# Performance work log

Measured on AMD Instinct MI355X. Metric: run time of the kernel, lower is better.

## Reference

```python
import jax, jax.numpy as jnp
import numpy as np

D_MODEL = 1024
N_EXPERTS = 8
TOP_K = 2


def setup_inputs() -> dict:
    key = jax.random.key(0)
    k1, k2, k3, k4 = jax.random.split(key, 4)
    B, S, D, E = 4, 2048, D_MODEL, N_EXPERTS
    dff = 4 * D
    # xavier-uniform style scale for expert weights
    lim = float(np.sqrt(6.0 / (D + dff)))
    return {
        "x": jax.random.normal(k1, (B, S, D), dtype=jnp.float32),
        "router_w": jax.random.normal(k2, (D, E), dtype=jnp.float32) * (1.0 / np.sqrt(D)),
        "router_b": jnp.zeros((E,), dtype=jnp.float32),
        "expert_up": jax.random.uniform(k3, (E, dff, D), dtype=jnp.float32, minval=-lim, maxval=lim),
        "expert_down": jax.random.uniform(k4, (E, D, dff), dtype=jnp.float32, minval=-lim, maxval=lim),
    }


def reference(x, router_w, router_b, expert_up, expert_down):
    B, S, D = x.shape
    E = expert_up.shape[0]
    x_flat = x.reshape(-1, D)                       # [T, D]
    logits = x_flat @ router_w + router_b           # [T, E]
    probs = jax.nn.softmax(logits, axis=-1)
    top_w, top_idx = jax.lax.top_k(probs, TOP_K)    # [T, K]
    # combine per-token top-k weights into a dense [T, E] combine matrix
    comb = jnp.sum(top_w[..., None] * jax.nn.one_hot(top_idx, E, dtype=x.dtype), axis=1)  # [T, E]
    output = jnp.zeros_like(x_flat)
    for e in range(E):  # fixed small expert count
        h = jax.nn.gelu(x_flat @ expert_up[e].T, approximate=False)   # [T, dff]
        out_e = h @ expert_down[e].T                                  # [T, D]
        output = output + comb[:, e:e + 1] * out_e
    return output.reshape(B, S, D)
```

## Files before the change

### kernel.cpp

```cpp
#include <hip/hip_runtime.h>
#include <hip/hip_bf16.h>
#include <cstdint>

#define T_TOK 8192
#define DM 1024
#define NE 8
#define DFF 4096

#define PERX_UP 576
#define PERX_DN 288

typedef __attribute__((ext_vector_type(8))) short bf16x8;
typedef __attribute__((ext_vector_type(4))) float f32x4;

__device__ __forceinline__ unsigned short f2bf(float f) {
  unsigned int b = __float_as_uint(f);
  b += 0x7FFFu + ((b >> 16) & 1u);
  return (unsigned short)(b >> 16);
}

__device__ __forceinline__ float gelu_exact(float v) {
  return 0.5f * v * (1.0f + erff(v * 0.70710678118654752440f));
}

__global__ void cvt_kernel(const float* __restrict__ x, unsigned short* __restrict__ xb) {
  size_t i = (size_t)blockIdx.x * blockDim.x + threadIdx.x;
  const f32x4* p = (const f32x4*)x;
  f32x4 a = p[2 * i];
  f32x4 b = p[2 * i + 1];
  union { bf16x8 v; unsigned short u[8]; } o;
  o.u[0] = f2bf(a.x); o.u[1] = f2bf(a.y); o.u[2] = f2bf(a.z); o.u[3] = f2bf(a.w);
  o.u[4] = f2bf(b.x); o.u[5] = f2bf(b.y); o.u[6] = f2bf(b.z); o.u[7] = f2bf(b.w);
  ((bf16x8*)xb)[i] = o.v;
}

__global__ void router_kernel(const float* __restrict__ x, const float* __restrict__ rw,
                              const float* __restrict__ rb, int* __restrict__ counts,
                              int* __restrict__ tlist, float* __restrict__ wlist) {
  const int lane = threadIdx.x & 63;
  const int t = blockIdx.x * 4 + (threadIdx.x >> 6);
  const float* xr = x + (size_t)t * DM;
  float acc[NE];
#pragma unroll
  for (int e = 0; e < NE; ++e) acc[e] = 0.0f;
#pragma unroll
  for (int i = 0; i < 16; ++i) {
    int d = lane + i * 64;
    float xv = xr[d];
    const float* wr = rw + (size_t)d * NE;
#pragma unroll
    for (int e = 0; e < NE; ++e) acc[e] = fmaf(xv, wr[e], acc[e]);
  }
#pragma unroll
  for (int off = 32; off; off >>= 1) {
#pragma unroll
    for (int e = 0; e < NE; ++e) acc[e] += __shfl_xor(acc[e], off);
  }
  float m = -1e30f;
#pragma unroll
  for (int e = 0; e < NE; ++e) { acc[e] += rb[e]; m = fmaxf(m, acc[e]); }
  float p[NE]; float s = 0.0f;
#pragma unroll
  for (int e = 0; e < NE; ++e) { p[e] = expf(acc[e] - m); s += p[e]; }
  int e1 = 0; float p1 = p[0];
#pragma unroll
  for (int e = 1; e < NE; ++e) if (p[e] > p1) { p1 = p[e]; e1 = e; }
  int e2 = -1; float p2 = -1e30f;
#pragma unroll
  for (int e = 0; e < NE; ++e) if (e != e1 && p[e] > p2) { p2 = p[e]; e2 = e; }
  float inv = 1.0f / s;
  if (lane == 0) {
    int r1 = atomicAdd(counts + e1, 1);
    tlist[e1 * T_TOK + r1] = t; wlist[e1 * T_TOK + r1] = p1 * inv;
    int r2 = atomicAdd(counts + e2, 1);
    tlist[e2 * T_TOK + r2] = t; wlist[e2 * T_TOK + r2] = p2 * inv;
  }
}

__global__ void prefix_kernel(const int* __restrict__ counts, int* __restrict__ offs,
                              int* __restrict__ wl_up, int* __restrict__ wl_dn) {
  __shared__ int te[144], tr[144], sn;
  if (threadIdx.x == 0) {
    int s = 0, n = 0;
    for (int e = 0; e < NE; ++e) {
      offs[e] = s; s += counts[e];
      int ntile = (counts[e] + 127) / 128;
      for (int r = 0; r < ntile; ++r) { te[n] = e; tr[n] = r; ++n; }
    }
    sn = n;
  }
  __syncthreads();
  const int n = sn;
  for (int idx = threadIdx.x; idx < 8 * PERX_UP; idx += blockDim.x) {
    int k = idx / PERX_UP, i = idx % PERX_UP;
    int g0 = (n * k) / 8, g1 = (n * (k + 1)) / 8, gc = g1 - g0;
    int v = -1;
    if (gc > 0 && i < 32 * gc) {
      int ct = i / gc, g = g0 + i % gc;
      v = (te[g] << 24) | (tr[g] << 16) | ct;
    }
    wl_up[idx] = v;
  }
  for (int idx = threadIdx.x; idx < 8 * PERX_DN; idx += blockDim.x) {
    int k = idx / PERX_DN, i = idx % PERX_DN;
    int g0 = (n * k) / 8, g1 = (n * (k + 1)) / 8, gc = g1 - g0;
    int v = -1;
    if (gc > 0 && i < 16 * gc) {
      int kh = i / (8 * gc);
      int rem = i % (8 * gc);
      int ct = rem / gc, g = g0 + rem % gc;
      v = (te[g] << 24) | (tr[g] << 16) | (kh << 8) | ct;
    }
    wl_dn[idx] = v;
  }
}

#define GL2LDS16(g, l) \
  __builtin_amdgcn_global_load_lds((const __attribute__((address_space(1))) unsigned int*)(g), \
                                   (__attribute__((address_space(3))) unsigned int*)(l), 16, 0, 0)

#define VMCNT4   asm volatile("s_waitcnt vmcnt(4)" ::: "memory")
#define VMCNT0   asm volatile("s_waitcnt vmcnt(0)" ::: "memory")
#define LGKM0    asm volatile("s_waitcnt lgkmcnt(0)" ::: "memory")
#define BARRIER() do { asm volatile("" ::: "memory"); __builtin_amdgcn_s_barrier(); asm volatile("" ::: "memory"); } while (0)

#define STAGE(bi, t) do { \
  const int k_ = (t) * 32; \
  GL2LDS16(asrc0 + k_, smem + (bi) * 4096 + wv * 512); \
  GL2LDS16(asrc1 + k_, smem + (bi) * 4096 + wv * 512 + 2048); \
  GL2LDS16(bsrc0 + k_, smem + 8192 + (bi) * 4096 + wv * 512); \
  GL2LDS16(bsrc1 + k_, smem + 8192 + (bi) * 4096 + wv * 512 + 2048); \
} while (0)

#define COMPUTE(bi) do { \
  const unsigned short* sA_ = smem + (bi) * 4096; \
  const unsigned short* sB_ = smem + 8192 + (bi) * 4096; \
  bf16x8 af_[4], bf_[4]; \
  _Pragma("unroll") \
  for (int m_ = 0; m_ < 4; ++m_) af_[m_] = *(const bf16x8*)(sA_ + (wr + m_ * 16 + lr) * 32 + kx); \
  _Pragma("unroll") \
  for (int n_ = 0; n_ < 4; ++n_) bf_[n_] = *(const bf16x8*)(sB_ + (wc + n_ * 16 + lr) * 32 + kx); \
  _Pragma("unroll") \
  for (int m_ = 0; m_ < 4; ++m_) \
    _Pragma("unroll") \
    for (int n_ = 0; n_ < 4; ++n_) \
      acc[m_][n_] = __builtin_amdgcn_mfma_f32_16x16x32_bf16(af_[m_], bf_[n_], acc[m_][n_], 0, 0, 0); \
} while (0)

#define KLOOP(NT) do { \
  STAGE(0, 0); \
  STAGE(1, 1); \
  for (int t = 0; t < (NT); ++t) { \
    const int b_ = t & 1; \
    if (t + 1 < (NT)) { VMCNT4; } else { VMCNT0; } \
    BARRIER(); \
    COMPUTE(b_); \
    if (t + 2 < (NT)) { \
      LGKM0; \
      BARRIER(); \
      STAGE(b_, t + 2); \
    } \
  } \
} while (0)

__global__ __launch_bounds__(256, 4) void gemm_up_kernel(
    const unsigned short* __restrict__ xb, const unsigned short* __restrict__ wb,
    const int* __restrict__ counts, const int* __restrict__ offs,
    const int* __restrict__ wl, const int* __restrict__ tlist,
    unsigned short* __restrict__ h) {
  const int xcd = blockIdx.x & 7, slot = blockIdx.x >> 3;
  const int item = wl[xcd * PERX_UP + slot];
  if (item < 0) return;
  const int e = (item >> 24) & 7, rt = (item >> 16) & 0xFF, ct = item & 0xFF;
  const int cnt = counts[e];

  __shared__ unsigned short smem[16384];

  const int tid = threadIdx.x;
  const int wv = tid >> 6, ln = tid & 63;
  const int swz = (tid & 3) ^ ((tid >> 3) & 3);

  const int arow = wv * 16 + (ln >> 2);
  int r0 = rt * 128 + arow;
  int r1 = r0 + 64;
  const int tok0 = tlist[e * T_TOK + (r0 < cnt ? r0 : cnt - 1)];
  const int tok1 = tlist[e * T_TOK + (r1 < cnt ? r1 : cnt - 1)];
  const unsigned short* asrc0 = xb + (size_t)tok0 * DM + swz * 8;
  const unsigned short* asrc1 = xb + (size_t)tok1 * DM + swz * 8;

  const unsigned short* bsrc0 =
      wb + (size_t)e * DFF * DM + (size_t)(ct * 128 + arow) * DM + swz * 8;
  const unsigned short* bsrc1 = bsrc0 + (size_t)64 * DM;

  const int wr = (wv >> 1) * 64, wc = (wv & 1) * 64;
  const int lr = ln & 15;
  const int kx = (((ln >> 4) ^ ((lr >> 1) & 3))) * 8;

  f32x4 acc[4][4] = {};

  KLOOP(DM / 32);

  BARRIER();

  unsigned short* sH = smem;
#pragma unroll
  for (int m = 0; m < 4; ++m) {
    int rloc = wr + m * 16 + (ln >> 4) * 4;
#pragma unroll
    for (int j = 0; j < 4; ++j) {
      int row = rloc + j;
#pragma unroll
      for (int n = 0; n < 4; ++n) {
        int col = wc + n * 16 + lr;
        int sl = ((col >> 3) ^ (row & 7)) * 8 + (col & 7);
        sH[row * 128 + sl] = f2bf(gelu_exact(acc[m][n][j]));
      }
    }
  }
  __syncthreads();
  const size_t hbase = (size_t)offs[e];
#pragma unroll
  for (int it = 0; it < 8; ++it) {
    int idx = it * 256 + tid;
    int row = idx >> 4, c8 = idx & 15;
    if (rt * 128 + row < cnt) {
      unsigned short* hp = h + (hbase + rt * 128 + row) * (size_t)DFF + ct * 128 + c8 * 8;
      *(bf16x8*)hp = *(const bf16x8*)&sH[row * 128 + (c8 ^ (row & 7)) * 8];
    }
  }
}

__global__ __launch_bounds__(256, 4) void gemm_down_kernel(
    const unsigned short* __restrict__ h, const unsigned short* __restrict__ wb,
    const int* __restrict__ counts, const int* __restrict__ offs,
    const int* __restrict__ wl, const int* __restrict__ tlist,
    const float* __restrict__ wlist, float* __restrict__ out) {
  const int xcd = blockIdx.x & 7, slot = blockIdx.x >> 3;
  const int item = wl[xcd * PERX_DN + slot];
  if (item < 0) return;
  const int e = (item >> 24) & 7, rt = (item >> 16) & 0xFF;
  const int kh = (item >> 8) & 1, ct = item & 0xFF;
  const int cnt = counts[e];

  __shared__ unsigned short smem[16384];

  const int tid = threadIdx.x;
  const int wv = tid >> 6, ln = tid & 63;
  const int swz = (tid & 3) ^ ((tid >> 3) & 3);
  const size_t hbase = (size_t)offs[e];
  const int kbase = kh * (DFF / 2);

  const int arow = wv * 16 + (ln >> 2);
  int r0 = rt * 128 + arow;
  int r1 = r0 + 64;
  const unsigned short* asrc0 =
      h + (hbase + (r0 < cnt ? r0 : cnt - 1)) * (size_t)DFF + kbase + swz * 8;
  const unsigned short* asrc1 =
      h + (hbase + (r1 < cnt ? r1 : cnt - 1)) * (size_t)DFF + kbase + swz * 8;

  const unsigned short* bsrc0 =
      wb + (size_t)e * DM * DFF + (size_t)(ct * 128 + arow) * DFF + kbase + swz * 8;
  const unsigned short* bsrc1 = bsrc0 + (size_t)64 * DFF;

  const int wr = (wv >> 1) * 64, wc = (wv & 1) * 64;
  const int lr = ln & 15;
  const int kx = (((ln >> 4) ^ ((lr >> 1) & 3))) * 8;

  f32x4 acc[4][4] = {};

  KLOOP(DFF / 2 / 32);

#pragma unroll
  for (int m = 0; m < 4; ++m) {
    int rloc = wr + m * 16 + (ln >> 4) * 4;
#pragma unroll
    for (int j = 0; j < 4; ++j) {
      int row = rt * 128 + rloc + j;
      if (row < cnt) {
        int tok = tlist[e * T_TOK + row];
        float w = wlist[e * T_TOK + row];
        float* op = out + (size_t)tok * DM + ct * 128 + wc + lr;
#pragma unroll
        for (int n = 0; n < 4; ++n) atomicAdd(op + n * 16, w * acc[m][n][j]);
      }
    }
  }
}

extern "C" void kernel_launch(void* const* d_in, const int* in_sizes, int n_in,
                              void* d_out, int out_size, void* d_ws, size_t ws_size,
                              hipStream_t stream) {
  const float* x  = (const float*)d_in[0];
  const float* rw = (const float*)d_in[1];
  const float* rb = (const float*)d_in[2];
  const float* up = (const float*)d_in[3];
  const float* dn = (const float*)d_in[4];
  float* out = (float*)d_out;
  char* ws = (char*)d_ws;

  int*   counts = (int*)(ws + 0);
  int*   offs   = (int*)(ws + 128);
  int*   wl_up  = (int*)(ws + 4096);
  int*   wl_dn  = (int*)(ws + 24576);
  int*   tlist  = (int*)(ws + 65536);
  float* wlist  = (float*)(ws + 65536 + 262144);
  unsigned short* xb = (unsigned short*)(ws + 589824);
  unsigned short* h  = (unsigned short*)(ws + 17367040);
  unsigned short* wbuf = (unsigned short*)(ws + 151584768);

  hipMemsetAsync(counts, 0, 64, stream);
  hipMemsetAsync(d_out, 0, (size_t)T_TOK * DM * sizeof(float), stream);

  cvt_kernel<<<dim3((T_TOK * DM / 8) / 256), 256, 0, stream>>>(x, xb);
  router_kernel<<<dim3(T_TOK / 4), 256, 0, stream>>>(x, rw, rb, counts, tlist, wlist);
  prefix_kernel<<<dim3(1), 256, 0, stream>>>(counts, offs, wl_up, wl_dn);

  cvt_kernel<<<dim3((NE * DFF * DM / 8) / 256), 256, 0, stream>>>(up, wbuf);
  gemm_up_kernel<<<dim3(8 * PERX_UP), 256, 0, stream>>>(xb, wbuf, counts, offs, wl_up, tlist, h);

  cvt_kernel<<<dim3((NE * DM * DFF / 8) / 256), 256, 0, stream>>>(dn, wbuf);
  gemm_down_kernel<<<dim3(8 * PERX_DN), 256, 0, stream>>>(h, wbuf, counts, offs, wl_dn, tlist, wlist, out);
}
```

Measured before the change: 700.6 us.

## Widen GEMM tiles to 128x256 and use triple-buffered LDS pipeline

Both expert GEMMs now compute 128x256 output tiles instead of 128x128, so each wave holds a 64x128 accumulator and the weight tile is reused across more tokens. The work lists are halved to match. The K loop moves from double to triple buffering, which lets one barrier per iteration replace the lgkmcnt wait plus second barrier before restaging. The cost is more LDS (72KB) and registers per block, with occupancy dropped to 2 blocks per CU, and fewer blocks to spread load across the device.

```diff
diff --git a/kernel.cpp b/kernel.cpp
--- a/kernel.cpp
+++ b/kernel.cpp
@@ -7,8 +7,8 @@
 #define NE 8
 #define DFF 4096
 
-#define PERX_UP 576
-#define PERX_DN 288
+#define PERX_UP 288
+#define PERX_DN 144
 
 typedef __attribute__((ext_vector_type(8))) short bf16x8;
 typedef __attribute__((ext_vector_type(4))) float f32x4;
@@ -95,7 +95,7 @@
     int k = idx / PERX_UP, i = idx % PERX_UP;
     int g0 = (n * k) / 8, g1 = (n * (k + 1)) / 8, gc = g1 - g0;
     int v = -1;
-    if (gc > 0 && i < 32 * gc) {
+    if (gc > 0 && i < 16 * gc) {
       int ct = i / gc, g = g0 + i % gc;
       v = (te[g] << 24) | (tr[g] << 16) | ct;
     }
@@ -105,9 +105,9 @@
     int k = idx / PERX_DN, i = idx % PERX_DN;
     int g0 = (n * k) / 8, g1 = (n * (k + 1)) / 8, gc = g1 - g0;
     int v = -1;
-    if (gc > 0 && i < 16 * gc) {
-      int kh = i / (8 * gc);
-      int rem = i % (8 * gc);
+    if (gc > 0 && i < 8 * gc) {
+      int kh = i / (4 * gc);
+      int rem = i % (4 * gc);
       int ct = rem / gc, g = g0 + rem % gc;
       v = (te[g] << 24) | (tr[g] << 16) | (kh << 8) | ct;
     }
@@ -119,51 +119,50 @@
   __builtin_amdgcn_global_load_lds((const __attribute__((address_space(1))) unsigned int*)(g), \
                                    (__attribute__((address_space(3))) unsigned int*)(l), 16, 0, 0)
 
-#define VMCNT4   asm volatile("s_waitcnt vmcnt(4)" ::: "memory")
+#define VMCNT6   asm volatile("s_waitcnt vmcnt(6)" ::: "memory")
 #define VMCNT0   asm volatile("s_waitcnt vmcnt(0)" ::: "memory")
-#define LGKM0    asm volatile("s_waitcnt lgkmcnt(0)" ::: "memory")
 #define BARRIER() do { asm volatile("" ::: "memory"); __builtin_amdgcn_s_barrier(); asm volatile("" ::: "memory"); } while (0)
 
 #define STAGE(bi, t) do { \
   const int k_ = (t) * 32; \
   GL2LDS16(asrc0 + k_, smem + (bi) * 4096 + wv * 512); \
-  GL2LDS16(asrc1 + k_, smem + (bi) * 4096 + wv * 512 + 2048); \
-  GL2LDS16(bsrc0 + k_, smem + 8192 + (bi) * 4096 + wv * 512); \
-  GL2LDS16(bsrc1 + k_, smem + 8192 + (bi) * 4096 + wv * 512 + 2048); \
+  GL2LDS16(asrc1 + k_, smem + (bi) * 4096 + 2048 + wv * 512); \
+  GL2LDS16(bsrc0 + k_, smem + 12288 + (bi) * 8192 + wv * 512); \
+  GL2LDS16(bsrc1 + k_, smem + 12288 + (bi) * 8192 + 2048 + wv * 512); \
+  GL2LDS16(bsrc2 + k_, smem + 12288 + (bi) * 8192 + 4096 + wv * 512); \
+  GL2LDS16(bsrc3 + k_, smem + 12288 + (bi) * 8192 + 6144 + wv * 512); \
 } while (0)
 
 #define COMPUTE(bi) do { \
   const unsigned short* sA_ = smem + (bi) * 4096; \
-  const unsigned short* sB_ = smem + 8192 + (bi) * 4096; \
-  bf16x8 af_[4], bf_[4]; \
+  const unsigned short* sB_ = smem + 12288 + (bi) * 8192; \
+  bf16x8 af_[4], bf_[8]; \
   _Pragma("unroll") \
   for (int m_ = 0; m_ < 4; ++m_) af_[m_] = *(const bf16x8*)(sA_ + (wr + m_ * 16 + lr) * 32 + kx); \
   _Pragma("unroll") \
-  for (int n_ = 0; n_ < 4; ++n_) bf_[n_] = *(const bf16x8*)(sB_ + (wc + n_ * 16 + lr) * 32 + kx); \
+  for (int n_ = 0; n_ < 8; ++n_) bf_[n_] = *(const bf16x8*)(sB_ + (wc + n_ * 16 + lr) * 32 + kx); \
   _Pragma("unroll") \
   for (int m_ = 0; m_ < 4; ++m_) \
     _Pragma("unroll") \
-    for (int n_ = 0; n_ < 4; ++n_) \
+    for (int n_ = 0; n_ < 8; ++n_) \
       acc[m_][n_] = __builtin_amdgcn_mfma_f32_16x16x32_bf16(af_[m_], bf_[n_], acc[m_][n_], 0, 0, 0); \
 } while (0)
 
 #define KLOOP(NT) do { \
   STAGE(0, 0); \
   STAGE(1, 1); \
+  int bc_ = 0, bs_ = 2; \
   for (int t = 0; t < (NT); ++t) { \
-    const int b_ = t & 1; \
-    if (t + 1 < (NT)) { VMCNT4; } else { VMCNT0; } \
+    if (t + 1 < (NT)) { VMCNT6; } else { VMCNT0; } \
     BARRIER(); \
-    COMPUTE(b_); \
-    if (t + 2 < (NT)) { \
-      LGKM0; \
-      BARRIER(); \
-      STAGE(b_, t + 2); \
-    } \
+    COMPUTE(bc_); \
+    if (t + 2 < (NT)) STAGE(bs_, t + 2); \
+    bc_ = (bc_ == 2) ? 0 : bc_ + 1; \
+    bs_ = (bs_ == 2) ? 0 : bs_ + 1; \
   } \
 } while (0)
 
-__global__ __launch_bounds__(256, 4) void gemm_up_kernel(
+__global__ __launch_bounds__(256, 2) void gemm_up_kernel(
     const unsigned short* __restrict__ xb, const unsigned short* __restrict__ wb,
     const int* __restrict__ counts, const int* __restrict__ offs,
     const int* __restrict__ wl, const int* __restrict__ tlist,
@@ -174,29 +173,30 @@
   const int e = (item >> 24) & 7, rt = (item >> 16) & 0xFF, ct = item & 0xFF;
   const int cnt = counts[e];
 
-  __shared__ unsigned short smem[16384];
+  __shared__ unsigned short smem[36864];
 
   const int tid = threadIdx.x;
   const int wv = tid >> 6, ln = tid & 63;
-  const int swz = (tid & 3) ^ ((tid >> 3) & 3);
-
-  const int arow = wv * 16 + (ln >> 2);
-  int r0 = rt * 128 + arow;
-  int r1 = r0 + 64;
-  const int tok0 = tlist[e * T_TOK + (r0 < cnt ? r0 : cnt - 1)];
-  const int tok1 = tlist[e * T_TOK + (r1 < cnt ? r1 : cnt - 1)];
+  const int srow = wv * 16 + (ln >> 2);
+  const int swz = (ln & 3) ^ ((ln >> 3) & 3);
+
+  int ra0 = rt * 128 + srow, ra1 = ra0 + 64;
+  const int tok0 = tlist[e * T_TOK + (ra0 < cnt ? ra0 : cnt - 1)];
+  const int tok1 = tlist[e * T_TOK + (ra1 < cnt ? ra1 : cnt - 1)];
   const unsigned short* asrc0 = xb + (size_t)tok0 * DM + swz * 8;
   const unsigned short* asrc1 = xb + (size_t)tok1 * DM + swz * 8;
 
   const unsigned short* bsrc0 =
-      wb + (size_t)e * DFF * DM + (size_t)(ct * 128 + arow) * DM + swz * 8;
+      wb + (size_t)e * DFF * DM + (size_t)(ct * 256 + srow) * DM + swz * 8;
   const unsigned short* bsrc1 = bsrc0 + (size_t)64 * DM;
-
-  const int wr = (wv >> 1) * 64, wc = (wv & 1) * 64;
+  const unsigned short* bsrc2 = bsrc0 + (size_t)128 * DM;
+  const unsigned short* bsrc3 = bsrc0 + (size_t)192 * DM;
+
+  const int wr = (wv >> 1) * 64, wc = (wv & 1) * 128;
   const int lr = ln & 15;
   const int kx = (((ln >> 4) ^ ((lr >> 1) & 3))) * 8;
 
-  f32x4 acc[4][4] = {};
+  f32x4 acc[4][8] = {};
 
   KLOOP(DM / 32);
 
@@ -210,27 +210,27 @@
     for (int j = 0; j < 4; ++j) {
       int row = rloc + j;
 #pragma unroll
-      for (int n = 0; n < 4; ++n) {
+      for (int n = 0; n < 8; ++n) {
         int col = wc + n * 16 + lr;
         int sl = ((col >> 3) ^ (row & 7)) * 8 + (col & 7);
-        sH[row * 128 + sl] = f2bf(gelu_exact(acc[m][n][j]));
+        sH[row * 256 + sl] = f2bf(gelu_exact(acc[m][n][j]));
       }
     }
   }
   __syncthreads();
   const size_t hbase = (size_t)offs[e];
 #pragma unroll
-  for (int it = 0; it < 8; ++it) {
+  for (int it = 0; it < 16; ++it) {
     int idx = it * 256 + tid;
-    int row = idx >> 4, c8 = idx & 15;
+    int row = idx >> 5, c8 = idx & 31;
     if (rt * 128 + row < cnt) {
-      unsigned short* hp = h + (hbase + rt * 128 + row) * (size_t)DFF + ct * 128 + c8 * 8;
-      *(bf16x8*)hp = *(const bf16x8*)&sH[row * 128 + (c8 ^ (row & 7)) * 8];
-    }
-  }
-}
-
-__global__ __launch_bounds__(256, 4) void gemm_down_kernel(
+      unsigned short* hp = h + (hbase + rt * 128 + row) * (size_t)DFF + ct * 256 + c8 * 8;
+      *(bf16x8*)hp = *(const bf16x8*)&sH[row * 256 + (c8 ^ (row & 7)) * 8];
+    }
+  }
+}
+
+__global__ __launch_bounds__(256, 2) void gemm_down_kernel(
     const unsigned short* __restrict__ h, const unsigned short* __restrict__ wb,
     const int* __restrict__ counts, const int* __restrict__ offs,
     const int* __restrict__ wl, const int* __restrict__ tlist,
@@ -242,31 +242,32 @@
   const int kh = (item >> 8) & 1, ct = item & 0xFF;
   const int cnt = counts[e];
 
-  __shared__ unsigned short smem[16384];
+  __shared__ unsigned short smem[36864];
 
   const int tid = threadIdx.x;
   const int wv = tid >> 6, ln = tid & 63;
-  const int swz = (tid & 3) ^ ((tid >> 3) & 3);
+  const int srow = wv * 16 + (ln >> 2);
+  const int swz = (ln & 3) ^ ((ln >> 3) & 3);
   const size_t hbase = (size_t)offs[e];
   const int kbase = kh * (DFF / 2);
 
-  const int arow = wv * 16 + (ln >> 2);
-  int r0 = rt * 128 + arow;
-  int r1 = r0 + 64;
+  int ra0 = rt * 128 + srow, ra1 = ra0 + 64;
   const unsigned short* asrc0 =
-      h + (hbase + (r0 < cnt ? r0 : cnt - 1)) * (size_t)DFF + kbase + swz * 8;
+      h + (hbase + (ra0 < cnt ? ra0 : cnt - 1)) * (size_t)DFF + kbase + swz * 8;
   const unsigned short* asrc1 =
-      h + (hbase + (r1 < cnt ? r1 : cnt - 1)) * (size_t)DFF + kbase + swz * 8;
+      h + (hbase + (ra1 < cnt ? ra1 : cnt - 1)) * (size_t)DFF + kbase + swz * 8;
 
   const unsigned short* bsrc0 =
-      wb + (size_t)e * DM * DFF + (size_t)(ct * 128 + arow) * DFF + kbase + swz * 8;
+      wb + (size_t)e * DM * DFF + (size_t)(ct * 256 + srow) * DFF + kbase + swz * 8;
   const unsigned short* bsrc1 = bsrc0 + (size_t)64 * DFF;
-
-  const int wr = (wv >> 1) * 64, wc = (wv & 1) * 64;
+  const unsigned short* bsrc2 = bsrc0 + (size_t)128 * DFF;
+  const unsigned short* bsrc3 = bsrc0 + (size_t)192 * DFF;
+
+  const int wr = (wv >> 1) * 64, wc = (wv & 1) * 128;
   const int lr = ln & 15;
   const int kx = (((ln >> 4) ^ ((lr >> 1) & 3))) * 8;
 
-  f32x4 acc[4][4] = {};
+  f32x4 acc[4][8] = {};
 
   KLOOP(DFF / 2 / 32);
 
@@ -279,9 +280,9 @@
       if (row < cnt) {
         int tok = tlist[e * T_TOK + row];
         float w = wlist[e * T_TOK + row];
-        float* op = out + (size_t)tok * DM + ct * 128 + wc + lr;
-#pragma unroll
-        for (int n = 0; n < 4; ++n) atomicAdd(op + n * 16, w * acc[m][n][j]);
+        float* op = out + (size_t)tok * DM + ct * 256 + wc + lr;
+#pragma unroll
+        for (int n = 0; n < 8; ++n) atomicAdd(op + n * 16, w * acc[m][n][j]);
       }
     }
   }
```

Measured after the change: 706.3 us. Within noise of the previous version (+0.8%).

## Enlarge GEMM tiles to 256x256 with 8 waves and 4-stage LDS pipeline

Applied to the files above, without the earlier changes.

Both expert GEMMs move from 128x128 tiles with 4 waves to 256x256 tiles with 8 waves per block, each wave computing a 128x64 sub-tile split into two MFMA halves. The K-loop becomes a 4-buffer pipeline that prefetches three stages ahead, issuing A and B loads separately between compute phases, and raises wave priority around the MFMA bursts. Work lists and routing tiles are resized to 256-row groups. The aim is higher arithmetic intensity and better overlap of global loads with MFMA, at the cost of 128KB of LDS per block, lower occupancy and coarser tiles that waste more on partially filled expert groups.

```diff
diff --git a/kernel.cpp b/kernel.cpp
--- a/kernel.cpp
+++ b/kernel.cpp
@@ -7,8 +7,8 @@
 #define NE 8
 #define DFF 4096
 
-#define PERX_UP 576
-#define PERX_DN 288
+#define PERX_UP 144
+#define PERX_DN 72
 
 typedef __attribute__((ext_vector_type(8))) short bf16x8;
 typedef __attribute__((ext_vector_type(4))) float f32x4;
@@ -79,12 +79,12 @@
 
 __global__ void prefix_kernel(const int* __restrict__ counts, int* __restrict__ offs,
                               int* __restrict__ wl_up, int* __restrict__ wl_dn) {
-  __shared__ int te[144], tr[144], sn;
+  __shared__ int te[80], tr[80], sn;
   if (threadIdx.x == 0) {
     int s = 0, n = 0;
     for (int e = 0; e < NE; ++e) {
       offs[e] = s; s += counts[e];
-      int ntile = (counts[e] + 127) / 128;
+      int ntile = (counts[e] + 255) / 256;
       for (int r = 0; r < ntile; ++r) { te[n] = e; tr[n] = r; ++n; }
     }
     sn = n;
@@ -95,7 +95,7 @@
     int k = idx / PERX_UP, i = idx % PERX_UP;
     int g0 = (n * k) / 8, g1 = (n * (k + 1)) / 8, gc = g1 - g0;
     int v = -1;
-    if (gc > 0 && i < 32 * gc) {
+    if (gc > 0 && i < 16 * gc) {
       int ct = i / gc, g = g0 + i % gc;
       v = (te[g] << 24) | (tr[g] << 16) | ct;
     }
@@ -105,9 +105,9 @@
     int k = idx / PERX_DN, i = idx % PERX_DN;
     int g0 = (n * k) / 8, g1 = (n * (k + 1)) / 8, gc = g1 - g0;
     int v = -1;
-    if (gc > 0 && i < 16 * gc) {
-      int kh = i / (8 * gc);
-      int rem = i % (8 * gc);
+    if (gc > 0 && i < 8 * gc) {
+      int kh = i / (4 * gc);
+      int rem = i % (4 * gc);
       int ct = rem / gc, g = g0 + rem % gc;
       v = (te[g] << 24) | (tr[g] << 16) | (kh << 8) | ct;
     }
@@ -119,51 +119,65 @@
   __builtin_amdgcn_global_load_lds((const __attribute__((address_space(1))) unsigned int*)(g), \
                                    (__attribute__((address_space(3))) unsigned int*)(l), 16, 0, 0)
 
+#define VMCNT8   asm volatile("s_waitcnt vmcnt(8)" ::: "memory")
 #define VMCNT4   asm volatile("s_waitcnt vmcnt(4)" ::: "memory")
 #define VMCNT0   asm volatile("s_waitcnt vmcnt(0)" ::: "memory")
 #define LGKM0    asm volatile("s_waitcnt lgkmcnt(0)" ::: "memory")
 #define BARRIER() do { asm volatile("" ::: "memory"); __builtin_amdgcn_s_barrier(); asm volatile("" ::: "memory"); } while (0)
 
-#define STAGE(bi, t) do { \
-  const int k_ = (t) * 32; \
-  GL2LDS16(asrc0 + k_, smem + (bi) * 4096 + wv * 512); \
-  GL2LDS16(asrc1 + k_, smem + (bi) * 4096 + wv * 512 + 2048); \
-  GL2LDS16(bsrc0 + k_, smem + 8192 + (bi) * 4096 + wv * 512); \
-  GL2LDS16(bsrc1 + k_, smem + 8192 + (bi) * 4096 + wv * 512 + 2048); \
+#define STAGE_A(b, t) do { const int k_ = (t) * 32; \
+  GL2LDS16(asrc0 + k_, smem + (b) * 8192 + tid * 8); \
+  GL2LDS16(asrc1 + k_, smem + (b) * 8192 + 4096 + tid * 8); \
 } while (0)
-
-#define COMPUTE(bi) do { \
-  const unsigned short* sA_ = smem + (bi) * 4096; \
-  const unsigned short* sB_ = smem + 8192 + (bi) * 4096; \
-  bf16x8 af_[4], bf_[4]; \
-  _Pragma("unroll") \
-  for (int m_ = 0; m_ < 4; ++m_) af_[m_] = *(const bf16x8*)(sA_ + (wr + m_ * 16 + lr) * 32 + kx); \
-  _Pragma("unroll") \
-  for (int n_ = 0; n_ < 4; ++n_) bf_[n_] = *(const bf16x8*)(sB_ + (wc + n_ * 16 + lr) * 32 + kx); \
-  _Pragma("unroll") \
-  for (int m_ = 0; m_ < 4; ++m_) \
-    _Pragma("unroll") \
-    for (int n_ = 0; n_ < 4; ++n_) \
-      acc[m_][n_] = __builtin_amdgcn_mfma_f32_16x16x32_bf16(af_[m_], bf_[n_], acc[m_][n_], 0, 0, 0); \
+#define STAGE_B(b, t) do { const int k_ = (t) * 32; \
+  GL2LDS16(bsrc0 + k_, smem + 32768 + (b) * 8192 + tid * 8); \
+  GL2LDS16(bsrc1 + k_, smem + 32768 + (b) * 8192 + 4096 + tid * 8); \
 } while (0)
 
 #define KLOOP(NT) do { \
-  STAGE(0, 0); \
-  STAGE(1, 1); \
+  STAGE_A(0, 0); STAGE_B(0, 0); \
+  STAGE_A(1, 1); STAGE_B(1, 1); \
+  STAGE_A(2, 2); STAGE_B(2, 2); \
+  VMCNT8; \
+  BARRIER(); \
   for (int t = 0; t < (NT); ++t) { \
-    const int b_ = t & 1; \
-    if (t + 1 < (NT)) { VMCNT4; } else { VMCNT0; } \
+    const int b_ = t & 3; \
+    const unsigned short* sAb = smem + b_ * 8192; \
+    const unsigned short* sBb = smem + 32768 + b_ * 8192; \
+    bf16x8 af_[4], bv_[4]; \
+     \
+    _Pragma("unroll") \
+    for (int m_ = 0; m_ < 4; ++m_) af_[m_] = *(const bf16x8*)(sAb + (wr + m_ * 16 + lr) * 32 + kx); \
+    _Pragma("unroll") \
+    for (int n_ = 0; n_ < 4; ++n_) bv_[n_] = *(const bf16x8*)(sBb + (wc + n_ * 16 + lr) * 32 + kx); \
+    if (t + 3 < (NT)) STAGE_A((t + 3) & 3, t + 3); \
+    BARRIER(); LGKM0; \
+    __builtin_amdgcn_s_setprio(1); \
+    _Pragma("unroll") \
+    for (int m_ = 0; m_ < 4; ++m_) \
+      _Pragma("unroll") \
+      for (int n_ = 0; n_ < 4; ++n_) \
+        acc[m_][n_] = __builtin_amdgcn_mfma_f32_16x16x32_bf16(af_[m_], bv_[n_], acc[m_][n_], 0, 0, 0); \
+    __builtin_amdgcn_s_setprio(0); \
     BARRIER(); \
-    COMPUTE(b_); \
-    if (t + 2 < (NT)) { \
-      LGKM0; \
-      BARRIER(); \
-      STAGE(b_, t + 2); \
-    } \
+     \
+    _Pragma("unroll") \
+    for (int m_ = 0; m_ < 4; ++m_) af_[m_] = *(const bf16x8*)(sAb + (wr + 64 + m_ * 16 + lr) * 32 + kx); \
+    if (t + 3 < (NT)) STAGE_B((t + 3) & 3, t + 3); \
+    if (t < (NT) - 3) { VMCNT8; } else if (t == (NT) - 3) { VMCNT4; } else { VMCNT0; } \
+    BARRIER(); LGKM0; \
+    __builtin_amdgcn_s_setprio(1); \
+    _Pragma("unroll") \
+    for (int m_ = 0; m_ < 4; ++m_) \
+      _Pragma("unroll") \
+      for (int n_ = 0; n_ < 4; ++n_) \
+        acc[m_ + 4][n_] = __builtin_amdgcn_mfma_f32_16x16x32_bf16(af_[m_], bv_[n_], acc[m_ + 4][n_], 0, 0, 0); \
+    __builtin_amdgcn_s_setprio(0); \
+    BARRIER(); \
   } \
 } while (0)
 
-__global__ __launch_bounds__(256, 4) void gemm_up_kernel(
+__global__ __launch_bounds__(512, 2) void gemm_up_kernel(
     const unsigned short* __restrict__ xb, const unsigned short* __restrict__ wb,
     const int* __restrict__ counts, const int* __restrict__ offs,
     const int* __restrict__ wl, const int* __restrict__ tlist,
@@ -174,38 +188,34 @@
   const int e = (item >> 24) & 7, rt = (item >> 16) & 0xFF, ct = item & 0xFF;
   const int cnt = counts[e];
 
-  __shared__ unsigned short smem[16384];
+  __shared__ unsigned short smem[65536];
 
   const int tid = threadIdx.x;
-  const int wv = tid >> 6, ln = tid & 63;
+  const int wid = tid >> 6, ln = tid & 63;
   const int swz = (tid & 3) ^ ((tid >> 3) & 3);
 
-  const int arow = wv * 16 + (ln >> 2);
-  int r0 = rt * 128 + arow;
-  int r1 = r0 + 64;
+  int r0 = rt * 256 + (tid >> 2), r1 = r0 + 128;
   const int tok0 = tlist[e * T_TOK + (r0 < cnt ? r0 : cnt - 1)];
   const int tok1 = tlist[e * T_TOK + (r1 < cnt ? r1 : cnt - 1)];
   const unsigned short* asrc0 = xb + (size_t)tok0 * DM + swz * 8;
   const unsigned short* asrc1 = xb + (size_t)tok1 * DM + swz * 8;
 
   const unsigned short* bsrc0 =
-      wb + (size_t)e * DFF * DM + (size_t)(ct * 128 + arow) * DM + swz * 8;
-  const unsigned short* bsrc1 = bsrc0 + (size_t)64 * DM;
-
-  const int wr = (wv >> 1) * 64, wc = (wv & 1) * 64;
-  const int lr = ln & 15;
-  const int kx = (((ln >> 4) ^ ((lr >> 1) & 3))) * 8;
-
-  f32x4 acc[4][4] = {};
+      wb + (size_t)e * DFF * DM + (size_t)(ct * 256 + (tid >> 2)) * DM + swz * 8;
+  const unsigned short* bsrc1 = bsrc0 + (size_t)128 * DM;
+
+  const int wr = (wid >> 2) * 128, wc = (wid & 3) * 64;
+  const int lr = ln & 15, g4 = ln >> 4;
+  const int kx = ((g4 ^ ((lr >> 1) & 3))) * 8;
+
+  f32x4 acc[8][4] = {};
 
   KLOOP(DM / 32);
 
-  BARRIER();
-
   unsigned short* sH = smem;
 #pragma unroll
-  for (int m = 0; m < 4; ++m) {
-    int rloc = wr + m * 16 + (ln >> 4) * 4;
+  for (int m = 0; m < 8; ++m) {
+    int rloc = wr + m * 16 + g4 * 4;
 #pragma unroll
     for (int j = 0; j < 4; ++j) {
       int row = rloc + j;
@@ -213,24 +223,24 @@
       for (int n = 0; n < 4; ++n) {
         int col = wc + n * 16 + lr;
         int sl = ((col >> 3) ^ (row & 7)) * 8 + (col & 7);
-        sH[row * 128 + sl] = f2bf(gelu_exact(acc[m][n][j]));
+        sH[row * 256 + sl] = f2bf(gelu_exact(acc[m][n][j]));
       }
     }
   }
   __syncthreads();
   const size_t hbase = (size_t)offs[e];
 #pragma unroll
-  for (int it = 0; it < 8; ++it) {
-    int idx = it * 256 + tid;
-    int row = idx >> 4, c8 = idx & 15;
-    if (rt * 128 + row < cnt) {
-      unsigned short* hp = h + (hbase + rt * 128 + row) * (size_t)DFF + ct * 128 + c8 * 8;
-      *(bf16x8*)hp = *(const bf16x8*)&sH[row * 128 + (c8 ^ (row & 7)) * 8];
-    }
-  }
-}
-
-__global__ __launch_bounds__(256, 4) void gemm_down_kernel(
+  for (int it = 0; it < 16; ++it) {
+    int idx = it * 512 + tid;
+    int row = idx >> 5, c8 = idx & 31;
+    if (rt * 256 + row < cnt) {
+      unsigned short* hp = h + (hbase + rt * 256 + row) * (size_t)DFF + ct * 256 + c8 * 8;
+      *(bf16x8*)hp = *(const bf16x8*)&sH[row * 256 + (c8 ^ (row & 7)) * 8];
+    }
+  }
+}
+
+__global__ __launch_bounds__(512, 2) void gemm_down_kernel(
     const unsigned short* __restrict__ h, const unsigned short* __restrict__ wb,
     const int* __restrict__ counts, const int* __restrict__ offs,
     const int* __restrict__ wl, const int* __restrict__ tlist,
@@ -242,44 +252,42 @@
   const int kh = (item >> 8) & 1, ct = item & 0xFF;
   const int cnt = counts[e];
 
-  __shared__ unsigned short smem[16384];
+  __shared__ unsigned short smem[65536];
 
   const int tid = threadIdx.x;
-  const int wv = tid >> 6, ln = tid & 63;
+  const int wid = tid >> 6, ln = tid & 63;
   const int swz = (tid & 3) ^ ((tid >> 3) & 3);
   const size_t hbase = (size_t)offs[e];
   const int kbase = kh * (DFF / 2);
 
-  const int arow = wv * 16 + (ln >> 2);
-  int r0 = rt * 128 + arow;
-  int r1 = r0 + 64;
+  int r0 = rt * 256 + (tid >> 2), r1 = r0 + 128;
   const unsigned short* asrc0 =
       h + (hbase + (r0 < cnt ? r0 : cnt - 1)) * (size_t)DFF + kbase + swz * 8;
   const unsigned short* asrc1 =
       h + (hbase + (r1 < cnt ? r1 : cnt - 1)) * (size_t)DFF + kbase + swz * 8;
 
   const unsigned short* bsrc0 =
-      wb + (size_t)e * DM * DFF + (size_t)(ct * 128 + arow) * DFF + kbase + swz * 8;
-  const unsigned short* bsrc1 = bsrc0 + (size_t)64 * DFF;
-
-  const int wr = (wv >> 1) * 64, wc = (wv & 1) * 64;
-  const int lr = ln & 15;
-  const int kx = (((ln >> 4) ^ ((lr >> 1) & 3))) * 8;
-
-  f32x4 acc[4][4] = {};
+      wb + (size_t)e * DM * DFF + (size_t)(ct * 256 + (tid >> 2)) * DFF + kbase + swz * 8;
+  const unsigned short* bsrc1 = bsrc0 + (size_t)128 * DFF;
+
+  const int wr = (wid >> 2) * 128, wc = (wid & 3) * 64;
+  const int lr = ln & 15, g4 = ln >> 4;
+  const int kx = ((g4 ^ ((lr >> 1) & 3))) * 8;
+
+  f32x4 acc[8][4] = {};
 
   KLOOP(DFF / 2 / 32);
 
 #pragma unroll
-  for (int m = 0; m < 4; ++m) {
-    int rloc = wr + m * 16 + (ln >> 4) * 4;
+  for (int m = 0; m < 8; ++m) {
+    int rloc = wr + m * 16 + g4 * 4;
 #pragma unroll
     for (int j = 0; j < 4; ++j) {
-      int row = rt * 128 + rloc + j;
+      int row = rt * 256 + rloc + j;
       if (row < cnt) {
         int tok = tlist[e * T_TOK + row];
         float w = wlist[e * T_TOK + row];
-        float* op = out + (size_t)tok * DM + ct * 128 + wc + lr;
+        float* op = out + (size_t)tok * DM + ct * 256 + wc + lr;
 #pragma unroll
         for (int n = 0; n < 4; ++n) atomicAdd(op + n * 16, w * acc[m][n][j]);
       }
@@ -316,8 +324,8 @@
   prefix_kernel<<<dim3(1), 256, 0, stream>>>(counts, offs, wl_up, wl_dn);
 
   cvt_kernel<<<dim3((NE * DFF * DM / 8) / 256), 256, 0, stream>>>(up, wbuf);
-  gemm_up_kernel<<<dim3(8 * PERX_UP), 256, 0, stream>>>(xb, wbuf, counts, offs, wl_up, tlist, h);
+  gemm_up_kernel<<<dim3(8 * PERX_UP), 512, 0, stream>>>(xb, wbuf, counts, offs, wl_up, tlist, h);
 
   cvt_kernel<<<dim3((NE * DM * DFF / 8) / 256), 256, 0, stream>>>(dn, wbuf);
-  gemm_down_kernel<<<dim3(8 * PERX_DN), 256, 0, stream>>>(h, wbuf, counts, offs, wl_dn, tlist, wlist, out);
-}
+  gemm_down_kernel<<<dim3(8 * PERX_DN), 512, 0, stream>>>(h, wbuf, counts, offs, wl_dn, tlist, wlist, out);
+}
```

After: 806.2 us. 15.1% more time.

## Fuse conversion and router kernels and overlap down-weight conversion with up GEMM

Applied to the files above, without the earlier changes.

Merges the x conversion, up-weight conversion and router into a single launch using block-index ranges. It also appends extra blocks to the up-projection GEMM that convert the down-projection weights into a separate workspace buffer, so that conversion can overlap the GEMM tail. This removes launch gaps and serialization between kernels. The overlap path only runs when the workspace is large enough; otherwise the code falls back to a separate conversion launch. The extra blocks may compete with GEMM blocks for bandwidth and occupancy, and they shift the XCD round-robin mapping only for blocks beyond the GEMM range.

```diff
diff --git a/kernel.cpp b/kernel.cpp
--- a/kernel.cpp
+++ b/kernel.cpp
@@ -9,6 +9,11 @@
 
 #define PERX_UP 576
 #define PERX_DN 288
+#define GEMM_UP_BLOCKS (8 * PERX_UP)
+
+#define CVTX_BLOCKS 4096
+#define CVTW_BLOCKS 16384
+#define ROUT_BLOCKS 2048
 
 typedef __attribute__((ext_vector_type(8))) short bf16x8;
 typedef __attribute__((ext_vector_type(4))) float f32x4;
@@ -23,22 +28,37 @@
   return 0.5f * v * (1.0f + erff(v * 0.70710678118654752440f));
 }
 
-__global__ void cvt_kernel(const float* __restrict__ x, unsigned short* __restrict__ xb) {
-  size_t i = (size_t)blockIdx.x * blockDim.x + threadIdx.x;
-  const f32x4* p = (const f32x4*)x;
+__device__ __forceinline__ void cvt8(const float* __restrict__ src, unsigned short* __restrict__ dst,
+                                     size_t i) {
+  const f32x4* p = (const f32x4*)src;
   f32x4 a = p[2 * i];
   f32x4 b = p[2 * i + 1];
   union { bf16x8 v; unsigned short u[8]; } o;
   o.u[0] = f2bf(a.x); o.u[1] = f2bf(a.y); o.u[2] = f2bf(a.z); o.u[3] = f2bf(a.w);
   o.u[4] = f2bf(b.x); o.u[5] = f2bf(b.y); o.u[6] = f2bf(b.z); o.u[7] = f2bf(b.w);
-  ((bf16x8*)xb)[i] = o.v;
-}
-
-__global__ void router_kernel(const float* __restrict__ x, const float* __restrict__ rw,
-                              const float* __restrict__ rb, int* __restrict__ counts,
-                              int* __restrict__ tlist, float* __restrict__ wlist) {
+  ((bf16x8*)dst)[i] = o.v;
+}
+
+__global__ void cvt_kernel(const float* __restrict__ x, unsigned short* __restrict__ xb) {
+  cvt8(x, xb, (size_t)blockIdx.x * blockDim.x + threadIdx.x);
+}
+
+__global__ void fused_pre_kernel(const float* __restrict__ x, unsigned short* __restrict__ xb,
+                                 const float* __restrict__ up, unsigned short* __restrict__ upb,
+                                 const float* __restrict__ rw, const float* __restrict__ rb,
+                                 int* __restrict__ counts, int* __restrict__ tlist,
+                                 float* __restrict__ wlist) {
+  const int bid = blockIdx.x;
+  if (bid < CVTX_BLOCKS) {
+    cvt8(x, xb, (size_t)bid * 256 + threadIdx.x);
+    return;
+  }
+  if (bid < CVTX_BLOCKS + CVTW_BLOCKS) {
+    cvt8(up, upb, (size_t)(bid - CVTX_BLOCKS) * 256 + threadIdx.x);
+    return;
+  }
   const int lane = threadIdx.x & 63;
-  const int t = blockIdx.x * 4 + (threadIdx.x >> 6);
+  const int t = (bid - CVTX_BLOCKS - CVTW_BLOCKS) * 4 + (threadIdx.x >> 6);
   const float* xr = x + (size_t)t * DM;
   float acc[NE];
 #pragma unroll
@@ -167,7 +187,12 @@
     const unsigned short* __restrict__ xb, const unsigned short* __restrict__ wb,
     const int* __restrict__ counts, const int* __restrict__ offs,
     const int* __restrict__ wl, const int* __restrict__ tlist,
-    unsigned short* __restrict__ h) {
+    unsigned short* __restrict__ h,
+    const float* __restrict__ dn_f32, unsigned short* __restrict__ dn_bf16) {
+  if ((int)blockIdx.x >= GEMM_UP_BLOCKS) {
+    cvt8(dn_f32, dn_bf16, (size_t)(blockIdx.x - GEMM_UP_BLOCKS) * 256 + threadIdx.x);
+    return;
+  }
   const int xcd = blockIdx.x & 7, slot = blockIdx.x >> 3;
   const int item = wl[xcd * PERX_UP + slot];
   if (item < 0) return;
@@ -304,20 +329,29 @@
   int*   wl_dn  = (int*)(ws + 24576);
   int*   tlist  = (int*)(ws + 65536);
   float* wlist  = (float*)(ws + 65536 + 262144);
-  unsigned short* xb = (unsigned short*)(ws + 589824);
-  unsigned short* h  = (unsigned short*)(ws + 17367040);
-  unsigned short* wbuf = (unsigned short*)(ws + 151584768);
+  unsigned short* xb    = (unsigned short*)(ws + 589824);
+  unsigned short* h     = (unsigned short*)(ws + 17367040);
+  unsigned short* wbufA = (unsigned short*)(ws + 151584768);
+  unsigned short* wbufB = (unsigned short*)(ws + 218693632);
+  const bool big_ws = (ws_size >= (size_t)218693632 + 67108864);
 
   hipMemsetAsync(counts, 0, 64, stream);
   hipMemsetAsync(d_out, 0, (size_t)T_TOK * DM * sizeof(float), stream);
 
-  cvt_kernel<<<dim3((T_TOK * DM / 8) / 256), 256, 0, stream>>>(x, xb);
-  router_kernel<<<dim3(T_TOK / 4), 256, 0, stream>>>(x, rw, rb, counts, tlist, wlist);
+  fused_pre_kernel<<<dim3(CVTX_BLOCKS + CVTW_BLOCKS + ROUT_BLOCKS), 256, 0, stream>>>(
+      x, xb, up, wbufA, rw, rb, counts, tlist, wlist);
   prefix_kernel<<<dim3(1), 256, 0, stream>>>(counts, offs, wl_up, wl_dn);
 
-  cvt_kernel<<<dim3((NE * DFF * DM / 8) / 256), 256, 0, stream>>>(up, wbuf);
-  gemm_up_kernel<<<dim3(8 * PERX_UP), 256, 0, stream>>>(xb, wbuf, counts, offs, wl_up, tlist, h);
-
-  cvt_kernel<<<dim3((NE * DM * DFF / 8) / 256), 256, 0, stream>>>(dn, wbuf);
-  gemm_down_kernel<<<dim3(8 * PERX_DN), 256, 0, stream>>>(h, wbuf, counts, offs, wl_dn, tlist, wlist, out);
-}
+  if (big_ws) {
+    gemm_up_kernel<<<dim3(GEMM_UP_BLOCKS + CVTW_BLOCKS), 256, 0, stream>>>(
+        xb, wbufA, counts, offs, wl_up, tlist, h, dn, wbufB);
+    gemm_down_kernel<<<dim3(8 * PERX_DN), 256, 0, stream>>>(
+        h, wbufB, counts, offs, wl_dn, tlist, wlist, out);
+  } else {
+    gemm_up_kernel<<<dim3(GEMM_UP_BLOCKS), 256, 0, stream>>>(
+        xb, wbufA, counts, offs, wl_up, tlist, h, dn, wbufA);
+    cvt_kernel<<<dim3(CVTW_BLOCKS), 256, 0, stream>>>(dn, (unsigned short*)wbufA);
+    gemm_down_kernel<<<dim3(8 * PERX_DN), 256, 0, stream>>>(
+        h, wbufA, counts, offs, wl_dn, tlist, wlist, out);
+  }
+}
```

New measurement: 681.4 us. 2.7% less time.
